# Kernel optimization log

Hardware: AMD Instinct MI355X
Metric: run time of the kernel (lower is better)

## Reference

```python
import jax, jax.numpy as jnp
import numpy as np

B, C, H, W = 4, 64, 160, 160
K = 3
KK = K * K
PAD = (K - 1) // 2
EPS = 1e-5


def conv2d(x, w, b):
    y = jax.lax.conv_general_dilated(
        x, w, (1, 1), [(PAD, PAD), (PAD, PAD)],
        dimension_numbers=('NCHW', 'OIHW', 'NCHW'))
    return y + b[None, :, None, None]


def batchnorm(x, g, b, m, v):
    # eval-mode BN with running stats
    return (x - m[None, :, None, None]) * jax.lax.rsqrt(v + EPS)[None, :, None, None] * g[None, :, None, None] + b[None, :, None, None]


def bilinear_gather(x, py, px):
    # x: [B,C,H,W]; py,px: [B,KK,H,W] float sample coords -> [B,C,KK,H,W]
    Bx, Cx, Hx, Wx = x.shape
    y0 = jnp.floor(py)
    x0 = jnp.floor(px)
    ly = py - y0
    lx = px - x0
    x_flat = x.reshape(Bx, Cx, 1, Hx * Wx)
    acc = jnp.zeros((Bx, Cx, py.shape[1], Hx * Wx), dtype=x.dtype)
    corners = ((y0, x0, (1 - ly) * (1 - lx)),
               (y0, x0 + 1, (1 - ly) * lx),
               (y0 + 1, x0, ly * (1 - lx)),
               (y0 + 1, x0 + 1, ly * lx))
    for yi, xi, wgt in corners:
        valid = (yi >= 0) & (yi < Hx) & (xi >= 0) & (xi < Wx)
        yc = jnp.clip(yi, 0, Hx - 1).astype(jnp.int32)
        xc = jnp.clip(xi, 0, Wx - 1).astype(jnp.int32)
        idx = (yc * Wx + xc).reshape(Bx, -1, Hx * Wx)          # [B,KK,HW]
        g = jnp.take_along_axis(x_flat, idx[:, None], axis=3)  # [B,C,KK,HW]
        acc = acc + (wgt * valid).reshape(Bx, 1, -1, Hx * Wx) * g
    return acc.reshape(Bx, Cx, -1, Hx, Wx)


def modulated_deform_conv(x, offset, mask, weight):
    # x:[B,C,H,W] offset:[B,2*KK,H,W] (mmcv layout: pairs (dy,dx) interleaved) mask:[B,KK,H,W]
    Bx, Cx, Hx, Wx = x.shape
    Co = weight.shape[0]
    off = offset.reshape(Bx, KK, 2, Hx, Wx)
    k = jnp.arange(KK)
    ki = (k // K).astype(x.dtype)
    kj = (k % K).astype(x.dtype)
    ys = jnp.arange(Hx, dtype=x.dtype)
    xs = jnp.arange(Wx, dtype=x.dtype)
    py = ys[None, None, :, None] - PAD + ki[None, :, None, None] + off[:, :, 0]
    px = xs[None, None, None, :] - PAD + kj[None, :, None, None] + off[:, :, 1]
    samp = bilinear_gather(x, py, px)            # [B,C,KK,H,W]
    samp = samp * mask[:, None]                  # modulation
    return jnp.einsum('bckhw,ock->bohw', samp, weight.reshape(Co, Cx, KK))


def setup_inputs() -> dict:
    key = jax.random.key(0)
    ks = jax.random.split(key, 16)
    inp = {
        'x': jax.random.normal(ks[0], (B, C, H, W), jnp.float32),
        'w_om1': jax.random.normal(ks[1], (3 * KK, C, K, K), jnp.float32) * 0.01,
        'b_om1': jax.random.normal(ks[2], (3 * KK,), jnp.float32) * 0.01,
        'w_dcn1': jax.random.normal(ks[3], (C, C, K, K), jnp.float32) * 0.04,
        'bn1_g': jax.random.uniform(ks[4], (C,), jnp.float32, 0.5, 1.5),
        'bn1_b': jax.random.normal(ks[5], (C,), jnp.float32) * 0.1,
        'bn1_m': jax.random.normal(ks[6], (C,), jnp.float32) * 0.1,
        'bn1_v': jax.random.uniform(ks[7], (C,), jnp.float32, 0.5, 1.5),
        'w_om2': jax.random.normal(ks[8], (3 * KK, C, K, K), jnp.float32) * 0.01,
        'b_om2': jax.random.normal(ks[9], (3 * KK,), jnp.float32) * 0.01,
        'w_dcn2': jax.random.normal(ks[10], (C, C, K, K), jnp.float32) * 0.04,
        'bn2_g': jax.random.uniform(ks[11], (C,), jnp.float32, 0.5, 1.5),
        'bn2_b': jax.random.normal(ks[12], (C,), jnp.float32) * 0.1,
        'bn2_m': jax.random.normal(ks[13], (C,), jnp.float32) * 0.1,
        'bn2_v': jax.random.uniform(ks[14], (C,), jnp.float32, 0.5, 1.5),
    }
    return inp


def reference(x, w_om1, b_om1, w_dcn1, bn1_g, bn1_b, bn1_m, bn1_v,
              w_om2, b_om2, w_dcn2, bn2_g, bn2_b, bn2_m, bn2_v):
    identity = x
    om1 = conv2d(x, w_om1, b_om1)
    o1, o2, m1 = jnp.split(om1, 3, axis=1)
    offset1 = jnp.concatenate([o1, o2], axis=1)
    mask1 = jax.nn.sigmoid(m1)
    out = modulated_deform_conv(x, offset1, mask1, w_dcn1)
    out = batchnorm(out, bn1_g, bn1_b, bn1_m, bn1_v)
    out = jax.nn.gelu(out, approximate=False)
    om2 = conv2d(out, w_om2, b_om2)
    o1b, o2b, m2 = jnp.split(om2, 3, axis=1)
    offset2 = jnp.concatenate([o1b, o2b], axis=1)
    mask2 = jax.nn.sigmoid(m2)
    out = modulated_deform_conv(out, offset2, mask2, w_dcn2)
    out = batchnorm(out, bn2_g, bn2_b, bn2_m, bn2_v)
    out = out + identity
    return jax.nn.gelu(out, approximate=False)
```

## Files before the change

### kernel.cpp

```cpp
#include <hip/hip_runtime.h>
#include <math.h>

#define HH 160
#define WW 160
#define HWSZ 25600
#define TR 14
#define TC 22
#define NSLOT 308

typedef __attribute__((ext_vector_type(8))) short short8;
typedef __attribute__((ext_vector_type(4))) short short4v;
typedef __attribute__((ext_vector_type(8))) _Float16 half8;
typedef __attribute__((ext_vector_type(2))) _Float16 half2v;
typedef __attribute__((ext_vector_type(4))) float f32x4;
typedef __attribute__((ext_vector_type(16))) float f32x16;

__device__ __forceinline__ short f2h(float f) {
  union { _Float16 h; short s; } u; u.h = (_Float16)f; return u.s;
}
__device__ __forceinline__ float h2f(short s) {
  union { _Float16 h; short s; } u; u.s = s; return (float)u.h;
}
__device__ __forceinline__ half2v bcast_h(short s) {
  unsigned int x = (unsigned short)s; x |= x << 16;
  union { unsigned int u; half2v h; } v; v.u = x; return v.h;
}

__global__ __launch_bounds__(256) void pre_kernel(
    const float* __restrict__ x,
    const float* __restrict__ g1, const float* __restrict__ b1,
    const float* __restrict__ m1, const float* __restrict__ v1,
    const float* __restrict__ g2, const float* __restrict__ b2,
    const float* __restrict__ m2, const float* __restrict__ v2,
    const float* __restrict__ wd1, const float* __restrict__ wd2,
    const float* __restrict__ wo1, const float* __restrict__ wo2,
    float* __restrict__ sc, short* __restrict__ wd1h, short* __restrict__ wd2h,
    short* __restrict__ wo1h, short* __restrict__ wo2h,
    short* __restrict__ xcl) {
  __shared__ short tmp[64][72];
  int t = threadIdx.x;
  int bx = blockIdx.x;
  if (bx < 1600) {
    int b = bx / 400, p0 = (bx - b * 400) * 64;
    const float* xb = x + (size_t)b * 64 * HWSZ;
    for (int i = t; i < 4096; i += 256) {
      int c = i >> 6, p = i & 63;
      tmp[p][c] = f2h(xb[c * HWSZ + p0 + p]);
    }
    __syncthreads();
    short* ob = xcl + ((size_t)b * HWSZ + p0) * 64;
    for (int i = t; i < 512; i += 256) {
      int p = i >> 3, g = i & 7;
      *(short8*)&ob[p * 64 + g * 8] = *(const short8*)&tmp[p][g * 8];
    }
    return;
  }
  int i0 = (bx - 1600) * 256 + t;
  for (int i = i0; i < 36864; i += 16384) {
    int j = i & 7, oc = (i >> 3) & 31, hi = (i >> 8) & 1;
    int ot = (i >> 9) & 1, s = (i >> 10) & 3, tap = i >> 12;
    int src = (ot * 32 + oc) * 576 + (s * 16 + hi * 8 + j) * 9 + tap;
    wd1h[i] = f2h(wd1[src]);
    wd2h[i] = f2h(wd2[src]);
  }
  for (int i = i0; i < 18432; i += 16384) {
    int j = i & 7, q = (i >> 3) & 3, m = (i >> 5) & 15;
    int ot = (i >> 9) & 1, f = i >> 10;
    int kp = f * 32 + q * 8 + j;
    int k = kp >> 6, c = kp & 63;
    int oc = ot * 16 + m;
    wo1h[i] = (oc < 27) ? f2h(wo1[oc * 576 + c * 9 + k]) : (short)0;
    wo2h[i] = (oc < 27) ? f2h(wo2[oc * 576 + c * 9 + k]) : (short)0;
  }
  if (i0 < 64) {
    float s1 = g1[i0] * rsqrtf(v1[i0] + 1e-5f);
    sc[i0]       = s1;
    sc[64 + i0]  = b1[i0] - m1[i0] * s1;
    float s2 = g2[i0] * rsqrtf(v2[i0] + 1e-5f);
    sc[128 + i0] = s2;
    sc[192 + i0] = b2[i0] - m2[i0] * s2;
  }
}

__global__ __launch_bounds__(256, 3) void dcn_fused(
    const short* __restrict__ xcl,
    const short* __restrict__ who,
    const float* __restrict__ bias_om,
    const short* __restrict__ whd,
    const float* __restrict__ scale, const float* __restrict__ shift,
    const short* __restrict__ id_cl,
    short* __restrict__ out_cl,
    float* __restrict__ out_f32) {
  __shared__ short xt[NSLOT * 64];
  __shared__ __align__(16) short oms[5120];

  int t = threadIdx.x;
  int x0 = blockIdx.x * 16, y0 = blockIdx.y * 8, b = blockIdx.z;
  int w = t >> 6, lane = t & 63, q = lane >> 4, m = lane & 15;
  int hi = lane >> 5, p31 = lane & 31;
  int ybase = y0 - 3, xbase = x0 - 3;

  const short* xb = xcl + (size_t)b * HWSZ * 64;
  for (int i = t; i < NSLOT * 8; i += 256) {
    int slot = i >> 3, g = i & 7;
    int ty = slot / TC, tx = slot - ty * TC;
    int gy = ybase + ty, gx = xbase + tx;
    short8 v = {};
    if (gy >= 0 && gy < HH && gx >= 0 && gx < WW)
      v = *(const short8*)&xb[(gy * WW + gx) * 64 + g * 8];
    *(short8*)&xt[slot * 64 + ((g ^ (slot & 7)) << 3)] = v;
  }
  __syncthreads();

  {
    f32x4 oacc[2][2] = {};
#pragma unroll 6
    for (int f = 0; f < 18; f++) {
      int k = f >> 1;
      int ki = k / 3, kj = k - ki * 3;
      int g = (f & 1) * 4 + q;
      const short* ap = who + (f * 128 + m * 4 + q) * 8;
      short8 a0 = *(const short8*)ap;
      short8 a1 = *(const short8*)(ap + 512);
      union { short8 s8; half8 h; } A0, A1;
      A0.s8 = a0; A1.s8 = a1;
#pragma unroll
      for (int p = 0; p < 2; p++) {
        int slotb = (w * 2 + p + ki + 2) * TC + (m + kj + 2);
        union { short8 s8; half8 h; } B;
        B.s8 = *(const short8*)&xt[slotb * 64 + ((g ^ (slotb & 7)) << 3)];
        oacc[p][0] = __builtin_amdgcn_mfma_f32_16x16x32_f16(A0.h, B.h, oacc[p][0], 0, 0, 0);
        oacc[p][1] = __builtin_amdgcn_mfma_f32_16x16x32_f16(A1.h, B.h, oacc[p][1], 0, 0, 0);
      }
    }
#pragma unroll
    for (int p = 0; p < 2; p++) {
      int px = w * 32 + p * 16 + m;
#pragma unroll
      for (int mt = 0; mt < 2; mt++) {
        short4v pv;
#pragma unroll
        for (int r = 0; r < 4; r++) {
          int oc = mt * 16 + q * 4 + r;
          float bb = (oc < 27) ? bias_om[oc] : 0.f;
          pv[r] = f2h(oacc[p][mt][r] + bb);
        }
        *(short4v*)&oms[px * 40 + mt * 16 + q * 4] = pv;
      }
    }
  }
  __syncthreads();

  union { short s[40]; short8 v8[5]; } omr;
  {
    int px = w * 32 + p31;
#pragma unroll
    for (int i = 0; i < 5; i++)
      omr.v8[i] = *(const short8*)&oms[px * 40 + i * 8];
  }

  int y = y0 + w * 2 + (p31 >> 4), x = x0 + m;

  short4v ivs[8];
  if (out_f32) {
    size_t pbase = ((size_t)b * HWSZ + y * WW + x) * 64;
#pragma unroll
    for (int ot = 0; ot < 2; ot++)
#pragma unroll
      for (int blk = 0; blk < 4; blk++)
        ivs[ot * 4 + blk] =
            *(const short4v*)&id_cl[pbase + ot * 32 + blk * 8 + hi * 4];
  }

  f32x16 acc0 = {}, acc1 = {};
#pragma unroll
  for (int k = 0; k < 9; ++k) {
    float dy = h2f(omr.s[2 * k]);
    float dx = h2f(omr.s[2 * k + 1]);
    float ml = h2f(omr.s[18 + k]);
    float msk = 1.f / (1.f + __expf(-ml));
    int ki = k / 3, kj = k - ki * 3;
    float py  = (float)(y - 1 + ki) + dy;
    float pxf = (float)(x - 1 + kj) + dx;
    float fy = floorf(py), fx = floorf(pxf);
    float ly = py - fy, lx = pxf - fx;
    int yi0 = (int)fy, xi0 = (int)fx;
    bool vy0 = (yi0 >= 0) & (yi0 < HH), vy1 = (yi0 + 1 >= 0) & (yi0 + 1 < HH);
    bool vx0 = (xi0 >= 0) & (xi0 < WW), vx1 = (xi0 + 1 >= 0) & (xi0 + 1 < WW);
    int ty0 = min(max(yi0 - ybase, 0), TR - 2);
    int tx0 = min(max(xi0 - xbase, 0), TC - 2);
    int p00 = ty0 * TC + tx0;
    half2v w00 = bcast_h(f2h((vy0 & vx0) ? (1.f - ly) * (1.f - lx) * msk : 0.f));
    half2v w01 = bcast_h(f2h((vy0 & vx1) ? (1.f - ly) * lx * msk : 0.f));
    half2v w10 = bcast_h(f2h((vy1 & vx0) ? ly * (1.f - lx) * msk : 0.f));
    half2v w11 = bcast_h(f2h((vy1 & vx1) ? ly * lx * msk : 0.f));
    int s00 = p00, s01 = p00 + 1, s10 = p00 + TC, s11 = p00 + TC + 1;
#pragma unroll
    for (int s = 0; s < 4; s++) {
      int g = s * 2 + hi;
      union { short8 s8; half2v h[4]; } c00, c01, c10, c11, bb;
      c00.s8 = *(const short8*)&xt[s00 * 64 + ((g ^ (s00 & 7)) << 3)];
      c01.s8 = *(const short8*)&xt[s01 * 64 + ((g ^ (s01 & 7)) << 3)];
      c10.s8 = *(const short8*)&xt[s10 * 64 + ((g ^ (s10 & 7)) << 3)];
      c11.s8 = *(const short8*)&xt[s11 * 64 + ((g ^ (s11 & 7)) << 3)];
#pragma unroll
      for (int d = 0; d < 4; d++)
        bb.h[d] = c00.h[d] * w00 + c01.h[d] * w01 + c10.h[d] * w10 +
                  c11.h[d] * w11;
      const short* ap = whd + k * 4096 + s * 1024 + lane * 8;
      short8 a0 = *(const short8*)ap;
      short8 a1 = *(const short8*)(ap + 512);
      union { short8 s8; half8 h8; } B, A0, A1;
      B.s8 = bb.s8; A0.s8 = a0; A1.s8 = a1;
      acc0 = __builtin_amdgcn_mfma_f32_32x32x16_f16(A0.h8, B.h8, acc0, 0, 0, 0);
      acc1 = __builtin_amdgcn_mfma_f32_32x32x16_f16(A1.h8, B.h8, acc1, 0, 0, 0);
    }
  }

  if (out_f32) {
#pragma unroll
    for (int ot = 0; ot < 2; ot++) {
#pragma unroll
      for (int r = 0; r < 16; r++) {
        int oc = ot * 32 + (r & 3) + 8 * (r >> 2) + 4 * hi;
        float a = ot ? acc1[r] : acc0[r];
        size_t idx = ((size_t)(b * 64 + oc)) * HWSZ + y * WW + x;
        float v = a * scale[oc] + shift[oc] + h2f(ivs[ot * 4 + (r >> 2)][r & 3]);
        v = 0.5f * v * (1.f + erff(v * 0.70710678118654752f));
        out_f32[idx] = v;
      }
    }
  } else {
    size_t base = ((size_t)b * HWSZ + y * WW + x) * 64;
#pragma unroll
    for (int ot = 0; ot < 2; ot++) {
#pragma unroll
      for (int blk = 0; blk < 4; blk++) {
        short4v pv;
#pragma unroll
        for (int rr = 0; rr < 4; rr++) {
          int r = blk * 4 + rr;
          int oc = ot * 32 + blk * 8 + hi * 4 + rr;
          float a = ot ? acc1[r] : acc0[r];
          float v = a * scale[oc] + shift[oc];
          v = 0.5f * v * (1.f + erff(v * 0.70710678118654752f));
          pv[rr] = f2h(v);
        }
        *(short4v*)&out_cl[base + ot * 32 + blk * 8 + hi * 4] = pv;
      }
    }
  }
}

extern "C" void kernel_launch(void* const* d_in, const int* in_sizes, int n_in,
                              void* d_out, int out_size, void* d_ws, size_t ws_size,
                              hipStream_t stream) {
  const float* x     = (const float*)d_in[0];
  const float* w_om1 = (const float*)d_in[1];
  const float* b_om1 = (const float*)d_in[2];
  const float* w_d1  = (const float*)d_in[3];
  const float* bn1g  = (const float*)d_in[4];
  const float* bn1b  = (const float*)d_in[5];
  const float* bn1m  = (const float*)d_in[6];
  const float* bn1v  = (const float*)d_in[7];
  const float* w_om2 = (const float*)d_in[8];
  const float* b_om2 = (const float*)d_in[9];
  const float* w_d2  = (const float*)d_in[10];
  const float* bn2g  = (const float*)d_in[11];
  const float* bn2b  = (const float*)d_in[12];
  const float* bn2m  = (const float*)d_in[13];
  const float* bn2v  = (const float*)d_in[14];

  float* ws    = (float*)d_ws;
  float* sc    = ws;
  short* w1h   = (short*)(ws + 256);
  short* w2h   = w1h + 36864;
  short* wo1h  = w2h + 36864;
  short* wo2h  = wo1h + 18432;
  short* x_cl  = (short*)(ws + 55552);
  short* o1_cl = x_cl + 6553600;
  float* outp  = (float*)d_out;

  pre_kernel<<<dim3(1664), dim3(256), 0, stream>>>(
      x, bn1g, bn1b, bn1m, bn1v, bn2g, bn2b, bn2m, bn2v,
      w_d1, w_d2, w_om1, w_om2, sc, w1h, w2h, wo1h, wo2h, x_cl);

  dim3 grid(WW / 16, HH / 8, 4);
  dcn_fused<<<grid, dim3(256), 0, stream>>>(
      x_cl, wo1h, b_om1, w1h, sc, sc + 64, nullptr, o1_cl, nullptr);
  dcn_fused<<<grid, dim3(256), 0, stream>>>(
      o1_cl, wo2h, b_om2, w2h, sc + 128, sc + 192, x_cl, nullptr, outp);
}
```

Baseline: 196.2 us.

## Compute offset/mask conv with 32x32 MFMA and permlane swap instead of LDS

Switches the offset/mask convolution from 16x16x32 MFMAs to 32x32x16 MFMAs, with the weight prepack reordered so each lane loads its A fragment directly. The results are redistributed across lanes with permlane32_swap rather than written to a shared-memory staging buffer and read back after a barrier. This removes the oms LDS buffer and one __syncthreads, and occupancy is raised from 3 to 4 blocks per SM via launch bounds. It risks register pressure under the tighter bound and depends on the swap lane mapping matching the later consumers.

```diff
diff --git a/kernel.cpp b/kernel.cpp
--- a/kernel.cpp
+++ b/kernel.cpp
@@ -14,6 +14,7 @@
 typedef __attribute__((ext_vector_type(2))) _Float16 half2v;
 typedef __attribute__((ext_vector_type(4))) float f32x4;
 typedef __attribute__((ext_vector_type(16))) float f32x16;
+typedef __attribute__((ext_vector_type(2))) unsigned int uint2v;
 
 __device__ __forceinline__ short f2h(float f) {
   union { _Float16 h; short s; } u; u.h = (_Float16)f; return u.s;
@@ -64,13 +65,11 @@
     wd2h[i] = f2h(wd2[src]);
   }
   for (int i = i0; i < 18432; i += 16384) {
-    int j = i & 7, q = (i >> 3) & 3, m = (i >> 5) & 15;
-    int ot = (i >> 9) & 1, f = i >> 10;
-    int kp = f * 32 + q * 8 + j;
-    int k = kp >> 6, c = kp & 63;
-    int oc = ot * 16 + m;
-    wo1h[i] = (oc < 27) ? f2h(wo1[oc * 576 + c * 9 + k]) : (short)0;
-    wo2h[i] = (oc < 27) ? f2h(wo2[oc * 576 + c * 9 + k]) : (short)0;
+    int j = i & 7, oc = (i >> 3) & 31, hi = (i >> 8) & 1;
+    int s = (i >> 9) & 3, tap = i >> 11;
+    int src = oc * 576 + (s * 16 + hi * 8 + j) * 9 + tap;
+    wo1h[i] = (oc < 27) ? f2h(wo1[src]) : (short)0;
+    wo2h[i] = (oc < 27) ? f2h(wo2[src]) : (short)0;
   }
   if (i0 < 64) {
     float s1 = g1[i0] * rsqrtf(v1[i0] + 1e-5f);
@@ -82,7 +81,7 @@
   }
 }
 
-__global__ __launch_bounds__(256, 3) void dcn_fused(
+__global__ __launch_bounds__(256, 4) void dcn_fused(
     const short* __restrict__ xcl,
     const short* __restrict__ who,
     const float* __restrict__ bias_om,
@@ -92,11 +91,10 @@
     short* __restrict__ out_cl,
     float* __restrict__ out_f32) {
   __shared__ short xt[NSLOT * 64];
-  __shared__ __align__(16) short oms[5120];
 
   int t = threadIdx.x;
   int x0 = blockIdx.x * 16, y0 = blockIdx.y * 8, b = blockIdx.z;
-  int w = t >> 6, lane = t & 63, q = lane >> 4, m = lane & 15;
+  int w = t >> 6, lane = t & 63, m = lane & 15;
   int hi = lane >> 5, p31 = lane & 31;
   int ybase = y0 - 3, xbase = x0 - 3;
 
@@ -112,51 +110,35 @@
   }
   __syncthreads();
 
+  union { short s[32]; unsigned int u[16]; } omr;
   {
-    f32x4 oacc[2][2] = {};
-#pragma unroll 6
-    for (int f = 0; f < 18; f++) {
-      int k = f >> 1;
-      int ki = k / 3, kj = k - ki * 3;
-      int g = (f & 1) * 4 + q;
-      const short* ap = who + (f * 128 + m * 4 + q) * 8;
-      short8 a0 = *(const short8*)ap;
-      short8 a1 = *(const short8*)(ap + 512);
-      union { short8 s8; half8 h; } A0, A1;
-      A0.s8 = a0; A1.s8 = a1;
-#pragma unroll
-      for (int p = 0; p < 2; p++) {
-        int slotb = (w * 2 + p + ki + 2) * TC + (m + kj + 2);
-        union { short8 s8; half8 h; } B;
+    f32x16 oacc = {};
+#pragma unroll
+    for (int k9 = 0; k9 < 9; k9++) {
+      int ki = k9 / 3, kj = k9 - ki * 3;
+      int slotb = (w * 2 + (p31 >> 4) + ki + 2) * TC + ((p31 & 15) + kj + 2);
+#pragma unroll
+      for (int s = 0; s < 4; s++) {
+        int g = s * 2 + hi;
+        union { short8 s8; half8 h; } A, B;
         B.s8 = *(const short8*)&xt[slotb * 64 + ((g ^ (slotb & 7)) << 3)];
-        oacc[p][0] = __builtin_amdgcn_mfma_f32_16x16x32_f16(A0.h, B.h, oacc[p][0], 0, 0, 0);
-        oacc[p][1] = __builtin_amdgcn_mfma_f32_16x16x32_f16(A1.h, B.h, oacc[p][1], 0, 0, 0);
+        A.s8 = *(const short8*)&who[((k9 * 4 + s) * 64 + lane) * 8];
+        oacc = __builtin_amdgcn_mfma_f32_32x32x16_f16(A.h, B.h, oacc, 0, 0, 0);
       }
     }
 #pragma unroll
-    for (int p = 0; p < 2; p++) {
-      int px = w * 32 + p * 16 + m;
-#pragma unroll
-      for (int mt = 0; mt < 2; mt++) {
-        short4v pv;
-#pragma unroll
-        for (int r = 0; r < 4; r++) {
-          int oc = mt * 16 + q * 4 + r;
-          float bb = (oc < 27) ? bias_om[oc] : 0.f;
-          pv[r] = f2h(oacc[p][mt][r] + bb);
-        }
-        *(short4v*)&oms[px * 40 + mt * 16 + q * 4] = pv;
-      }
-    }
-  }
-  __syncthreads();
-
-  union { short s[40]; short8 v8[5]; } omr;
-  {
-    int px = w * 32 + p31;
-#pragma unroll
-    for (int i = 0; i < 5; i++)
-      omr.v8[i] = *(const short8*)&oms[px * 40 + i * 8];
+    for (int j = 0; j < 8; j++) {
+      int c0 = 2 * (j & 1) + 8 * (j >> 1);
+      int oc0 = c0 + 4 * hi;
+      float b0 = (oc0 < 27) ? bias_om[oc0] : 0.f;
+      float b1 = (oc0 + 1 < 27) ? bias_om[oc0 + 1] : 0.f;
+      union { unsigned int u; short s2[2]; } pk;
+      pk.s2[0] = f2h(oacc[2 * j] + b0);
+      pk.s2[1] = f2h(oacc[2 * j + 1] + b1);
+      uint2v sw = __builtin_amdgcn_permlane32_swap(pk.u, pk.u, false, false);
+      omr.u[c0 >> 1]       = sw[0];
+      omr.u[(c0 + 4) >> 1] = sw[1];
+    }
   }
 
   int y = y0 + w * 2 + (p31 >> 4), x = x0 + m;
```

Measured after the change: 183.2 us. -6.6%, faster.
